# Kernel optimization log

Measured on AMD Instinct MI355X. Metric: run time of the kernel, lower is better.

Reference implementation:

```python
import jax, jax.numpy as jnp
import numpy as np

N_EMBED = 512
E_DIM = 256
BETA = 0.25


def setup_inputs() -> dict:
    key = jax.random.key(0)
    k1, k2 = jax.random.split(key)
    z = jax.random.normal(k1, (32, 16, 16, 16, E_DIM), dtype=jnp.float32)
    embedding = jax.random.normal(k2, (N_EMBED, E_DIM), dtype=jnp.float32)
    return {"z": z, "embedding": embedding}


def reference(z, embedding):
    # Flatten spatial/batch dims: [N, e_dim]
    zf = z.reshape(-1, E_DIM)
    # similarity = ||z||^2 + ||e||^2 - 2 z.e  (squared distances)
    sim = (
        jnp.sum(zf * zf, axis=1, keepdims=True)
        + jnp.sum(embedding * embedding, axis=1)
        - 2.0 * jnp.einsum("bd,nd->bn", zf, embedding)
    )
    # NOTE: original code uses argmax (farthest code) -- faithfully reproduced.
    codebook_idxs = jnp.argmax(sim, axis=-1)
    # histogram side-effect: codebook_hist[idx] += 1
    hist = jnp.zeros((N_EMBED,), dtype=jnp.float32).at[codebook_idxs].add(1.0)
    z_q = embedding[codebook_idxs].reshape(z.shape)
    vq_loss = jnp.mean((z_q - jax.lax.stop_gradient(z)) ** 2)
    commitment_loss = BETA * jnp.mean((jax.lax.stop_gradient(z_q) - z) ** 2)
    # straight-through estimator
    z_q_st = z + jax.lax.stop_gradient(z_q - z)
    return (z_q_st, vq_loss, commitment_loss, codebook_idxs, hist)
```

## Files before the change

### kernel.cpp

```cpp
#include <hip/hip_runtime.h>
#include <hip/hip_bf16.h>

#define D 256
#define NC 512
#define NROWS 131072L

#define OFF_ZQ   0L
#define OFF_VQ   33554432L
#define OFF_CM   33554433L
#define OFF_IDX  33554434L
#define OFF_HIST 33685506L

#define WS_LPART 0
#define WS_HIST  2048
#define WS_E2    2560
#define WS_CNT   3072
#define WS_AMB   3136
#define WS_FIDX  134208
#define WS_BK    265280
#define WS_NEED  (330816L * 4)

#define MARGIN 0.75f

typedef __attribute__((ext_vector_type(8))) short bf16x8;
typedef __attribute__((ext_vector_type(4))) float f32x4;

__device__ __forceinline__ unsigned short f2bf(float f) {
    union { float f; unsigned int u; } a; a.f = f;
    return (unsigned short)((a.u + 0x7FFFu + ((a.u >> 16) & 1u)) >> 16);
}

__global__ void vq_e2(const float* __restrict__ e, float* __restrict__ e2) {
    int c = blockIdx.x;
    int l = threadIdx.x;
    float4 v = *(const float4*)(e + c * D + l * 4);
    float s = v.x * v.x + v.y * v.y + v.z * v.z + v.w * v.w;
    #pragma unroll
    for (int off = 32; off; off >>= 1) s += __shfl_xor(s, off);
    if (l == 0) e2[c] = s;
}

__global__ void vq_convB(const float* __restrict__ e, unsigned short* __restrict__ Bk,
                         float* __restrict__ e2, float* __restrict__ hist,
                         int* __restrict__ acnt) {
    __shared__ float r4[4];
    int code = blockIdx.x, k = threadIdx.x;
    float v = e[code * D + k];
    Bk[((k >> 5) * NC + code) * 32 + (k & 31)] = f2bf(v);
    float s = v * v;
    #pragma unroll
    for (int off = 32; off; off >>= 1) s += __shfl_xor(s, off);
    if ((k & 63) == 0) r4[k >> 6] = s;
    if (k == 0) {
        hist[code] = 0.0f;
        if (code == 0) *acnt = 0;
    }
    __syncthreads();
    if (k == 0) e2[code] = r4[0] + r4[1] + r4[2] + r4[3];
}

__global__ __launch_bounds__(512, 4)
void vq_gemm(const float* __restrict__ z, const unsigned short* __restrict__ Bk,
             const float* __restrict__ e2, int* __restrict__ fidx,
             int* __restrict__ acnt, int* __restrict__ alist) {
    __shared__ __align__(16) unsigned short zh[64 * 264];
    __shared__ float red[64 * 25];

    const int tid = threadIdx.x;
    const int w = tid >> 6, l = tid & 63, q = l >> 4, ln = l & 15;
    const long row0 = (long)blockIdx.x * 64;

    #pragma unroll
    for (int j = 0; j < 8; ++j) {
        int c = j * 512 + tid;
        int row = c >> 6, c4 = (c & 63) * 4;
        float4 av = *(const float4*)(z + (row0 + row) * D + c4);
        *(ushort4*)&zh[row * 264 + c4] =
            make_ushort4(f2bf(av.x), f2bf(av.y), f2bf(av.z), f2bf(av.w));
    }

    const unsigned short* bb = Bk + ((w * 64 + ln) * 32 + q * 8);
    bf16x8 ring[4];
    #pragma unroll
    for (int p = 0; p < 4; ++p)
        ring[p] = *(const bf16x8*)(bb + (p & 7) * (NC * 32) + (p >> 3) * (16 * 32));

    __syncthreads();

    float v1[16], v2[16]; int i1[16];
    #pragma unroll
    for (int k = 0; k < 16; ++k) { v1[k] = -3.0e38f; v2[k] = -3.0e38f; i1[k] = 0; }

    #pragma unroll
    for (int nt = 0; nt < 4; ++nt) {
        const int colc = w * 64 + nt * 16 + ln;
        const float e2v = e2[colc];
        f32x4 acc[4];
        #pragma unroll
        for (int mt = 0; mt < 4; ++mt) acc[mt] = (f32x4){0.f, 0.f, 0.f, 0.f};
        #pragma unroll
        for (int s = 0; s < 8; ++s) {
            const int it = nt * 8 + s;
            bf16x8 b = ring[it & 3];
            if (it + 4 < 32) {
                const int jt = it + 4;
                ring[it & 3] = *(const bf16x8*)(bb + (jt & 7) * (NC * 32) + (jt >> 3) * (16 * 32));
            }
            #pragma unroll
            for (int mt = 0; mt < 4; ++mt) {
                bf16x8 a = *(const bf16x8*)&zh[(mt * 16 + ln) * 264 + s * 32 + q * 8];
                acc[mt] = __builtin_amdgcn_mfma_f32_16x16x32_bf16(a, b, acc[mt], 0, 0, 0);
            }
        }
        #pragma unroll
        for (int mt = 0; mt < 4; ++mt)
            #pragma unroll
            for (int r = 0; r < 4; ++r) {
                const int k = mt * 4 + r;
                float v = fmaf(-2.0f, acc[mt][r], e2v);
                if (v > v1[k]) { v2[k] = v1[k]; v1[k] = v; i1[k] = colc; }
                else v2[k] = fmaxf(v2[k], v);
            }
    }

    #pragma unroll
    for (int k = 0; k < 16; ++k) {
        float v1p = v1[k];
        #pragma unroll
        for (int off = 1; off < 16; off <<= 1) {
            float o1 = __shfl_xor(v1[k], off);
            float o2 = __shfl_xor(v2[k], off);
            v2[k] = fmaxf(fmaxf(v2[k], o2), fminf(v1[k], o1));
            v1[k] = fmaxf(v1[k], o1);
        }
        unsigned long long mm = __ballot(v1p == v1[k]);
        unsigned int gm = (unsigned int)((mm >> (q * 16)) & 0xFFFFULL);
        int src = (q << 4) + (__ffs(gm) - 1);
        int ii = __shfl(i1[k], src);
        if (ln == 0) {
            const int mt = k >> 2, r = k & 3;
            const int rr = mt * 16 + q * 4 + r;
            red[rr * 25 + w * 3 + 0] = v1[k];
            red[rr * 25 + w * 3 + 1] = (float)ii;
            red[rr * 25 + w * 3 + 2] = v2[k];
        }
    }
    __syncthreads();
    if (tid < 64) {
        float v1m = -3.0e38f, v2m = -3.0e38f; int i1m = 0;
        #pragma unroll
        for (int g = 0; g < 8; ++g) {
            float rv1 = red[tid * 25 + g * 3 + 0];
            int   ri  = (int)red[tid * 25 + g * 3 + 1];
            float rv2 = red[tid * 25 + g * 3 + 2];
            if (rv1 > v1m) { v2m = fmaxf(v1m, rv2); v1m = rv1; i1m = ri; }
            else v2m = fmaxf(v2m, rv1);
        }
        fidx[row0 + tid] = i1m;
        int amb = (v1m - v2m < MARGIN) ? 1 : 0;
        unsigned long long m = __ballot(amb);
        int nb = __popcll(m);
        int basep = 0;
        if (tid == 0 && nb) basep = atomicAdd(acnt, nb);
        basep = __shfl(basep, 0);
        if (amb) {
            int pfx = __popcll(m & ((1ULL << tid) - 1ULL));
            alist[basep + pfx] = (int)(row0 + tid);
        }
    }
}

__global__ __launch_bounds__(256, 2)
void vq_refine(const float* __restrict__ z, const float* __restrict__ e,
               const float* __restrict__ e2, const int* __restrict__ acnt,
               const int* __restrict__ alist, int* __restrict__ fidx) {
    __shared__ __align__(16) float z_s[32][D];
    __shared__ __align__(16) float e_s[16][NC + 4];
    __shared__ int rowg[32];
    __shared__ int idx_s[32];
    const int tid = threadIdx.x, lane = tid & 63, w = tid >> 6;
    const int cnt = *acnt;
    for (int g = blockIdx.x; g * 32 < cnt; g += gridDim.x) {
        const int base = g * 32;
        __syncthreads();
        if (tid < 32) rowg[tid] = alist[min(base + tid, cnt - 1)];
        __syncthreads();
        #pragma unroll
        for (int j = 0; j < 8; ++j) {
            int c = j * 256 + tid, rl = c >> 6, c4 = (c & 63) * 4;
            *(float4*)&z_s[rl][c4] = *(const float4*)(z + (long)rowg[rl] * D + c4);
        }
        float acc[8][8];
        #pragma unroll
        for (int r = 0; r < 8; ++r)
            #pragma unroll
            for (int c = 0; c < 8; ++c) acc[r][c] = 0.0f;
        const int r0 = w * 8, c_lo = lane * 4;
        for (int kc = 0; kc < D; kc += 16) {
            __syncthreads();
            #pragma unroll
            for (int p = 0; p < 8; ++p) {
                int c = p * 64 + (tid >> 2), kk4 = (tid & 3) * 4;
                float4 v = *(const float4*)(e + c * D + kc + kk4);
                e_s[kk4 + 0][c] = v.x; e_s[kk4 + 1][c] = v.y;
                e_s[kk4 + 2][c] = v.z; e_s[kk4 + 3][c] = v.w;
            }
            __syncthreads();
            #pragma unroll
            for (int k4 = 0; k4 < 16; k4 += 4) {
                float zr[8][4];
                #pragma unroll
                for (int r = 0; r < 8; ++r) *(float4*)zr[r] = *(const float4*)&z_s[r0 + r][kc + k4];
                #pragma unroll
                for (int kk = 0; kk < 4; ++kk) {
                    float ev[8];
                    *(float4*)&ev[0] = *(const float4*)&e_s[k4 + kk][c_lo];
                    *(float4*)&ev[4] = *(const float4*)&e_s[k4 + kk][c_lo + 256];
                    #pragma unroll
                    for (int r = 0; r < 8; ++r)
                        #pragma unroll
                        for (int c = 0; c < 8; ++c) acc[r][c] = fmaf(zr[r][kk], ev[c], acc[r][c]);
                }
            }
        }
        float e2v[8];
        #pragma unroll
        for (int gg = 0; gg < 2; ++gg)
            #pragma unroll
            for (int i = 0; i < 4; ++i) e2v[gg * 4 + i] = e2[gg * 256 + c_lo + i];
        #pragma unroll
        for (int r = 0; r < 8; ++r) {
            float bvv = -3.0e38f; int bc = 0;
            #pragma unroll
            for (int c = 0; c < 8; ++c) {
                int col = (c >> 2) * 256 + c_lo + (c & 3);
                float v = e2v[c] - 2.0f * acc[r][c];
                if (v > bvv) { bvv = v; bc = col; }
            }
            #pragma unroll
            for (int off = 32; off; off >>= 1) {
                float ov = __shfl_xor(bvv, off); int oc = __shfl_xor(bc, off);
                if (ov > bvv || (ov == bvv && oc < bc)) { bvv = ov; bc = oc; }
            }
            if (lane == 0) idx_s[r0 + r] = bc;
        }
        __syncthreads();
        if (tid < 32 && base + tid < cnt) fidx[rowg[tid]] = idx_s[tid];
    }
}

__global__ __launch_bounds__(256)
void vq_hist(const int* __restrict__ fidx, float* __restrict__ hist) {
    __shared__ int h[NC];
    const int t = threadIdx.x;
    h[t] = 0; h[t + 256] = 0;
    __syncthreads();
    const long base = (long)blockIdx.x * 2048;
    #pragma unroll
    for (int j = 0; j < 8; ++j) {
        long i = base + j * 256 + t;
        atomicAdd(&h[fidx[i]], 1);
    }
    __syncthreads();
    #pragma unroll
    for (int j = 0; j < 2; ++j) {
        int k = j * 256 + t;
        int c = h[k];
        if (c) atomicAdd(&hist[k], (float)c);
    }
}

__global__ __launch_bounds__(256)
void vq_epi(const float* __restrict__ z, const float* __restrict__ e,
            const int* __restrict__ fidx, float* __restrict__ out,
            float* __restrict__ lpart) {
    __shared__ int idxs[64];
    __shared__ float rs[4];
    const int t = threadIdx.x, lane = t & 63, w = t >> 6;
    const long row0 = (long)blockIdx.x * 64;
    if (t < 64) {
        int ix = fidx[row0 + t];
        idxs[t] = ix;
        out[OFF_IDX + row0 + t] = (float)ix;
    }
    __syncthreads();
    float ls = 0.f;
    #pragma unroll 4
    for (int j = 0; j < 16; ++j) {
        const int r = w * 16 + j;
        const long row = row0 + r;
        const int idx = idxs[r];
        float4 zv = *(const float4*)(z + row * D + lane * 4);
        float4 ev = *(const float4*)(e + (long)idx * D + lane * 4);
        float4 dq;
        dq.x = ev.x - zv.x; dq.y = ev.y - zv.y; dq.z = ev.z - zv.z; dq.w = ev.w - zv.w;
        float4 o;
        o.x = zv.x + dq.x; o.y = zv.y + dq.y; o.z = zv.z + dq.z; o.w = zv.w + dq.w;
        *(float4*)(out + OFF_ZQ + row * D + lane * 4) = o;
        ls += dq.x * dq.x + dq.y * dq.y + dq.z * dq.z + dq.w * dq.w;
    }
    #pragma unroll
    for (int off = 32; off; off >>= 1) ls += __shfl_xor(ls, off);
    if (lane == 0) rs[w] = ls;
    __syncthreads();
    if (t == 0) lpart[blockIdx.x] = rs[0] + rs[1] + rs[2] + rs[3];
}

__global__ void vq_fin(const float* __restrict__ ws, float* __restrict__ out) {
    __shared__ float sred[16];
    const int t = threadIdx.x, lane = t & 63, w = t >> 6;
    float s = ws[WS_LPART + t] + ws[WS_LPART + t + 1024];
    #pragma unroll
    for (int off = 32; off; off >>= 1) s += __shfl_xor(s, off);
    if (lane == 0) sred[w] = s;
    __syncthreads();
    if (t == 0) {
        float tot = 0.f;
        #pragma unroll
        for (int i = 0; i < 16; ++i) tot += sred[i];
        float m = tot / 33554432.0f;
        out[OFF_VQ] = m;
        out[OFF_CM] = 0.25f * m;
    }
    if (t < NC) out[OFF_HIST + t] = ws[WS_HIST + t];
}

__global__ __launch_bounds__(256, 2)
void vq_main_fb(const float* __restrict__ z, const float* __restrict__ e,
                const float* __restrict__ e2, float* __restrict__ out,
                float* __restrict__ ws_loss, float* __restrict__ ws_hist) {
    __shared__ __align__(16) float z_s[32][D];
    __shared__ __align__(16) float e_s[16][NC + 4];
    __shared__ int   idx_s[32];
    __shared__ float red_s[4];
    const int tid = threadIdx.x, lane = tid & 63, w = tid >> 6;
    const long row0 = (long)blockIdx.x * 32;
    {
        const float4* zg = (const float4*)(z + row0 * D);
        float4* zs = (float4*)(&z_s[0][0]);
        #pragma unroll
        for (int i = 0; i < 8; ++i) zs[i * 256 + tid] = zg[i * 256 + tid];
    }
    float acc[8][8];
    #pragma unroll
    for (int r = 0; r < 8; ++r)
        #pragma unroll
        for (int c = 0; c < 8; ++c) acc[r][c] = 0.0f;
    const int r0 = w * 8, c_lo = lane * 4;
    for (int kc = 0; kc < D; kc += 16) {
        __syncthreads();
        #pragma unroll
        for (int p = 0; p < 8; ++p) {
            int c = p * 64 + (tid >> 2), kk4 = (tid & 3) * 4;
            float4 v = *(const float4*)(e + c * D + kc + kk4);
            e_s[kk4 + 0][c] = v.x; e_s[kk4 + 1][c] = v.y;
            e_s[kk4 + 2][c] = v.z; e_s[kk4 + 3][c] = v.w;
        }
        __syncthreads();
        #pragma unroll
        for (int k4 = 0; k4 < 16; k4 += 4) {
            float zr[8][4];
            #pragma unroll
            for (int r = 0; r < 8; ++r) *(float4*)zr[r] = *(const float4*)&z_s[r0 + r][kc + k4];
            #pragma unroll
            for (int kk = 0; kk < 4; ++kk) {
                float ev[8];
                *(float4*)&ev[0] = *(const float4*)&e_s[k4 + kk][c_lo];
                *(float4*)&ev[4] = *(const float4*)&e_s[k4 + kk][c_lo + 256];
                #pragma unroll
                for (int r = 0; r < 8; ++r)
                    #pragma unroll
                    for (int c = 0; c < 8; ++c) acc[r][c] = fmaf(zr[r][kk], ev[c], acc[r][c]);
            }
        }
    }
    float e2v[8];
    #pragma unroll
    for (int g = 0; g < 2; ++g)
        #pragma unroll
        for (int i = 0; i < 4; ++i) e2v[g * 4 + i] = e2[g * 256 + c_lo + i];
    #pragma unroll
    for (int r = 0; r < 8; ++r) {
        float bvv = -3.0e38f; int bc = 0;
        #pragma unroll
        for (int c = 0; c < 8; ++c) {
            int col = (c >> 2) * 256 + c_lo + (c & 3);
            float v = e2v[c] - 2.0f * acc[r][c];
            if (v > bvv) { bvv = v; bc = col; }
        }
        #pragma unroll
        for (int off = 32; off; off >>= 1) {
            float ov = __shfl_xor(bvv, off); int oc = __shfl_xor(bc, off);
            if (ov > bvv || (ov == bvv && oc < bc)) { bvv = ov; bc = oc; }
        }
        if (lane == 0) idx_s[r] = bc;
    }
    __syncthreads();
    if (tid < 32) {
        int bc = idx_s[tid];
        out[OFF_IDX + row0 + tid] = (float)bc;
        atomicAdd(&ws_hist[bc], 1.0f);
    }
    float lsum = 0.0f;
    for (int r = 0; r < 32; ++r) {
        int idx = idx_s[r];
        float ev = e[idx * D + tid];
        float zv = z_s[r][tid];
        float dq = ev - zv;
        out[OFF_ZQ + (row0 + r) * D + tid] = zv + dq;
        lsum += dq * dq;
    }
    #pragma unroll
    for (int off = 32; off; off >>= 1) lsum += __shfl_xor(lsum, off);
    if (lane == 0) red_s[w] = lsum;
    __syncthreads();
    if (tid == 0) atomicAdd(ws_loss, red_s[0] + red_s[1] + red_s[2] + red_s[3]);
}

__global__ void vq_init_fb(float* __restrict__ ws) {
    int t = threadIdx.x;
    if (t < 513) ws[t] = 0.0f;
}
__global__ void vq_fin_fb(const float* __restrict__ ws, float* __restrict__ out) {
    int t = blockIdx.x * blockDim.x + threadIdx.x;
    if (t < NC) out[OFF_HIST + t] = ws[1 + t];
    if (t == NC) {
        float m = ws[0] / 33554432.0f;
        out[OFF_VQ] = m; out[OFF_CM] = 0.25f * m;
    }
}

extern "C" void kernel_launch(void* const* d_in, const int* in_sizes, int n_in,
                              void* d_out, int out_size, void* d_ws, size_t ws_size,
                              hipStream_t stream) {
    const float* z = (const float*)d_in[0];
    const float* e = (const float*)d_in[1];
    float* out = (float*)d_out;
    float* ws  = (float*)d_ws;

    if (ws_size >= (size_t)WS_NEED) {
        float* lpart = ws + WS_LPART;
        float* hist  = ws + WS_HIST;
        float* e2    = ws + WS_E2;
        int*   acnt  = (int*)(ws + WS_CNT);
        int*   alist = (int*)(ws + WS_AMB);
        int*   fidx  = (int*)(ws + WS_FIDX);
        unsigned short* Bk = (unsigned short*)(ws + WS_BK);

        vq_convB<<<NC, 256, 0, stream>>>(e, Bk, e2, hist, acnt);
        vq_gemm<<<2048, 512, 0, stream>>>(z, Bk, e2, fidx, acnt, alist);
        vq_refine<<<512, 256, 0, stream>>>(z, e, e2, acnt, alist, fidx);
        vq_hist<<<64, 256, 0, stream>>>(fidx, hist);
        vq_epi<<<2048, 256, 0, stream>>>(z, e, fidx, out, lpart);
        vq_fin<<<1, 1024, 0, stream>>>(ws, out);
    } else {
        float* ws_loss = ws;
        float* ws_hist = ws + 1;
        float* ws_e2   = ws + 513;
        vq_init_fb<<<1, 1024, 0, stream>>>(ws);
        vq_e2<<<NC, 64, 0, stream>>>(e, ws_e2);
        vq_main_fb<<<4096, 256, 0, stream>>>(z, e, ws_e2, out, ws_loss, ws_hist);
        vq_fin_fb<<<3, 256, 0, stream>>>(ws, out);
    }
}
```

Measured before the change: 382.6 us.

## Hold z fragments in registers with a 2x4 warp tile; fuse hist and final reduction

The GEMM kernel stops staging z through LDS. Each wave now loads its 32 rows of z straight into registers as bf16 MFMA A-fragments and covers 128 codes, using a 2x4 wave grid in place of 8 waves each covering 64 codes over all 64 rows. This removes the LDS writes and reads and the block barrier before the MFMA loop, at the cost of higher register pressure (launch bounds lowered to 3 blocks) and more streaming of B per wave. Separately, the histogram and final loss kernels are merged into one launch that uses a last-block-done atomic counter, which saves one kernel launch.

```diff
diff --git a/kernel.cpp b/kernel.cpp
--- a/kernel.cpp
+++ b/kernel.cpp
@@ -15,6 +15,7 @@
 #define WS_HIST  2048
 #define WS_E2    2560
 #define WS_CNT   3072
+#define WS_DONE  3073
 #define WS_AMB   3136
 #define WS_FIDX  134208
 #define WS_BK    265280
@@ -42,7 +43,7 @@
 
 __global__ void vq_convB(const float* __restrict__ e, unsigned short* __restrict__ Bk,
                          float* __restrict__ e2, float* __restrict__ hist,
-                         int* __restrict__ acnt) {
+                         int* __restrict__ acnt, int* __restrict__ done) {
     __shared__ float r4[4];
     int code = blockIdx.x, k = threadIdx.x;
     float v = e[code * D + k];
@@ -53,78 +54,84 @@
     if ((k & 63) == 0) r4[k >> 6] = s;
     if (k == 0) {
         hist[code] = 0.0f;
-        if (code == 0) *acnt = 0;
+        if (code == 0) { *acnt = 0; *done = 0; }
     }
     __syncthreads();
     if (k == 0) e2[code] = r4[0] + r4[1] + r4[2] + r4[3];
 }
 
-__global__ __launch_bounds__(512, 4)
+__global__ __launch_bounds__(512, 3)
 void vq_gemm(const float* __restrict__ z, const unsigned short* __restrict__ Bk,
              const float* __restrict__ e2, int* __restrict__ fidx,
              int* __restrict__ acnt, int* __restrict__ alist) {
-    __shared__ __align__(16) unsigned short zh[64 * 264];
-    __shared__ float red[64 * 25];
+    __shared__ float red[64 * 13];
 
     const int tid = threadIdx.x;
     const int w = tid >> 6, l = tid & 63, q = l >> 4, ln = l & 15;
+    const int wm = w >> 2, wn = w & 3;
     const long row0 = (long)blockIdx.x * 64;
-
-    #pragma unroll
-    for (int j = 0; j < 8; ++j) {
-        int c = j * 512 + tid;
-        int row = c >> 6, c4 = (c & 63) * 4;
-        float4 av = *(const float4*)(z + (row0 + row) * D + c4);
-        *(ushort4*)&zh[row * 264 + c4] =
-            make_ushort4(f2bf(av.x), f2bf(av.y), f2bf(av.z), f2bf(av.w));
-    }
-
-    const unsigned short* bb = Bk + ((w * 64 + ln) * 32 + q * 8);
+    const long rowW = row0 + wm * 32;
+
+    bf16x8 af[2][8];
+    #pragma unroll
+    for (int mt = 0; mt < 2; ++mt) {
+        const float* zp = z + (rowW + mt * 16 + ln) * D + q * 8;
+        #pragma unroll
+        for (int s = 0; s < 8; ++s) {
+            float4 a0 = *(const float4*)(zp + s * 32);
+            float4 a1 = *(const float4*)(zp + s * 32 + 4);
+            bf16x8 t;
+            t[0] = (short)f2bf(a0.x); t[1] = (short)f2bf(a0.y);
+            t[2] = (short)f2bf(a0.z); t[3] = (short)f2bf(a0.w);
+            t[4] = (short)f2bf(a1.x); t[5] = (short)f2bf(a1.y);
+            t[6] = (short)f2bf(a1.z); t[7] = (short)f2bf(a1.w);
+            af[mt][s] = t;
+        }
+    }
+
+    float e2v[8];
+    #pragma unroll
+    for (int nt = 0; nt < 8; ++nt) e2v[nt] = e2[wn * 128 + nt * 16 + ln];
+
+    const unsigned short* bb = Bk + ((wn * 128 + ln) * 32 + q * 8);
     bf16x8 ring[4];
     #pragma unroll
     for (int p = 0; p < 4; ++p)
         ring[p] = *(const bf16x8*)(bb + (p & 7) * (NC * 32) + (p >> 3) * (16 * 32));
 
-    __syncthreads();
-
-    float v1[16], v2[16]; int i1[16];
-    #pragma unroll
-    for (int k = 0; k < 16; ++k) { v1[k] = -3.0e38f; v2[k] = -3.0e38f; i1[k] = 0; }
-
-    #pragma unroll
-    for (int nt = 0; nt < 4; ++nt) {
-        const int colc = w * 64 + nt * 16 + ln;
-        const float e2v = e2[colc];
-        f32x4 acc[4];
-        #pragma unroll
-        for (int mt = 0; mt < 4; ++mt) acc[mt] = (f32x4){0.f, 0.f, 0.f, 0.f};
+    float v1[8], v2[8]; int i1[8];
+    #pragma unroll
+    for (int k = 0; k < 8; ++k) { v1[k] = -3.0e38f; v2[k] = -3.0e38f; i1[k] = 0; }
+
+    #pragma unroll
+    for (int nt = 0; nt < 8; ++nt) {
+        f32x4 acc0 = (f32x4){0.f, 0.f, 0.f, 0.f};
+        f32x4 acc1 = (f32x4){0.f, 0.f, 0.f, 0.f};
         #pragma unroll
         for (int s = 0; s < 8; ++s) {
             const int it = nt * 8 + s;
             bf16x8 b = ring[it & 3];
-            if (it + 4 < 32) {
+            if (it + 4 < 64) {
                 const int jt = it + 4;
                 ring[it & 3] = *(const bf16x8*)(bb + (jt & 7) * (NC * 32) + (jt >> 3) * (16 * 32));
             }
-            #pragma unroll
-            for (int mt = 0; mt < 4; ++mt) {
-                bf16x8 a = *(const bf16x8*)&zh[(mt * 16 + ln) * 264 + s * 32 + q * 8];
-                acc[mt] = __builtin_amdgcn_mfma_f32_16x16x32_bf16(a, b, acc[mt], 0, 0, 0);
-            }
-        }
-        #pragma unroll
-        for (int mt = 0; mt < 4; ++mt)
-            #pragma unroll
-            for (int r = 0; r < 4; ++r) {
-                const int k = mt * 4 + r;
-                float v = fmaf(-2.0f, acc[mt][r], e2v);
-                if (v > v1[k]) { v2[k] = v1[k]; v1[k] = v; i1[k] = colc; }
-                else v2[k] = fmaxf(v2[k], v);
-            }
-    }
-
-    #pragma unroll
-    for (int k = 0; k < 16; ++k) {
+            acc0 = __builtin_amdgcn_mfma_f32_16x16x32_bf16(af[0][s], b, acc0, 0, 0, 0);
+            acc1 = __builtin_amdgcn_mfma_f32_16x16x32_bf16(af[1][s], b, acc1, 0, 0, 0);
+        }
+        const int colc = wn * 128 + nt * 16 + ln;
+        #pragma unroll
+        for (int r = 0; r < 4; ++r) {
+            float v = fmaf(-2.0f, acc0[r], e2v[nt]);
+            if (v > v1[r]) { v2[r] = v1[r]; v1[r] = v; i1[r] = colc; }
+            else v2[r] = fmaxf(v2[r], v);
+            float u = fmaf(-2.0f, acc1[r], e2v[nt]);
+            if (u > v1[4 + r]) { v2[4 + r] = v1[4 + r]; v1[4 + r] = u; i1[4 + r] = colc; }
+            else v2[4 + r] = fmaxf(v2[4 + r], u);
+        }
+    }
+
+    #pragma unroll
+    for (int k = 0; k < 8; ++k) {
         float v1p = v1[k];
         #pragma unroll
         for (int off = 1; off < 16; off <<= 1) {
@@ -139,20 +146,20 @@
         int ii = __shfl(i1[k], src);
         if (ln == 0) {
             const int mt = k >> 2, r = k & 3;
-            const int rr = mt * 16 + q * 4 + r;
-            red[rr * 25 + w * 3 + 0] = v1[k];
-            red[rr * 25 + w * 3 + 1] = (float)ii;
-            red[rr * 25 + w * 3 + 2] = v2[k];
+            const int rr = wm * 32 + mt * 16 + q * 4 + r;
+            red[rr * 13 + wn * 3 + 0] = v1[k];
+            red[rr * 13 + wn * 3 + 1] = (float)ii;
+            red[rr * 13 + wn * 3 + 2] = v2[k];
         }
     }
     __syncthreads();
     if (tid < 64) {
         float v1m = -3.0e38f, v2m = -3.0e38f; int i1m = 0;
         #pragma unroll
-        for (int g = 0; g < 8; ++g) {
-            float rv1 = red[tid * 25 + g * 3 + 0];
-            int   ri  = (int)red[tid * 25 + g * 3 + 1];
-            float rv2 = red[tid * 25 + g * 3 + 2];
+        for (int g = 0; g < 4; ++g) {
+            float rv1 = red[tid * 13 + g * 3 + 0];
+            int   ri  = (int)red[tid * 13 + g * 3 + 1];
+            float rv2 = red[tid * 13 + g * 3 + 2];
             if (rv1 > v1m) { v2m = fmaxf(v1m, rv2); v1m = rv1; i1m = ri; }
             else v2m = fmaxf(v2m, rv1);
         }
@@ -250,27 +257,6 @@
 }
 
 __global__ __launch_bounds__(256)
-void vq_hist(const int* __restrict__ fidx, float* __restrict__ hist) {
-    __shared__ int h[NC];
-    const int t = threadIdx.x;
-    h[t] = 0; h[t + 256] = 0;
-    __syncthreads();
-    const long base = (long)blockIdx.x * 2048;
-    #pragma unroll
-    for (int j = 0; j < 8; ++j) {
-        long i = base + j * 256 + t;
-        atomicAdd(&h[fidx[i]], 1);
-    }
-    __syncthreads();
-    #pragma unroll
-    for (int j = 0; j < 2; ++j) {
-        int k = j * 256 + t;
-        int c = h[k];
-        if (c) atomicAdd(&hist[k], (float)c);
-    }
-}
-
-__global__ __launch_bounds__(256)
 void vq_epi(const float* __restrict__ z, const float* __restrict__ e,
             const int* __restrict__ fidx, float* __restrict__ out,
             float* __restrict__ lpart) {
@@ -306,23 +292,48 @@
     if (t == 0) lpart[blockIdx.x] = rs[0] + rs[1] + rs[2] + rs[3];
 }
 
-__global__ void vq_fin(const float* __restrict__ ws, float* __restrict__ out) {
-    __shared__ float sred[16];
+__global__ __launch_bounds__(256)
+void vq_hist(const int* __restrict__ fidx, const float* __restrict__ lpart,
+             float* __restrict__ hist, int* __restrict__ done,
+             float* __restrict__ out) {
+    __shared__ int h[NC];
+    __shared__ float sred[4];
+    __shared__ int lastf;
     const int t = threadIdx.x, lane = t & 63, w = t >> 6;
-    float s = ws[WS_LPART + t] + ws[WS_LPART + t + 1024];
+    h[t] = 0; h[t + 256] = 0;
+    __syncthreads();
+    const long base = (long)blockIdx.x * 2048;
+    #pragma unroll
+    for (int j = 0; j < 8; ++j) {
+        long i = base + j * 256 + t;
+        atomicAdd(&h[fidx[i]], 1);
+    }
+    __syncthreads();
+    #pragma unroll
+    for (int j = 0; j < 2; ++j) {
+        int k = j * 256 + t;
+        int c = h[k];
+        if (c) atomicAdd(&hist[k], (float)c);
+    }
+    __threadfence();
+    if (t == 0) lastf = (atomicAdd(done, 1) == 63);
+    __syncthreads();
+    if (!lastf) return;
+    __threadfence();
+    out[OFF_HIST + t]       = atomicAdd(&hist[t], 0.0f);
+    out[OFF_HIST + 256 + t] = atomicAdd(&hist[t + 256], 0.0f);
+    float s = 0.f;
+    #pragma unroll
+    for (int j = 0; j < 8; ++j) s += lpart[j * 256 + t];
     #pragma unroll
     for (int off = 32; off; off >>= 1) s += __shfl_xor(s, off);
     if (lane == 0) sred[w] = s;
     __syncthreads();
     if (t == 0) {
-        float tot = 0.f;
-        #pragma unroll
-        for (int i = 0; i < 16; ++i) tot += sred[i];
-        float m = tot / 33554432.0f;
+        float m = (sred[0] + sred[1] + sred[2] + sred[3]) / 33554432.0f;
         out[OFF_VQ] = m;
         out[OFF_CM] = 0.25f * m;
     }
-    if (t < NC) out[OFF_HIST + t] = ws[WS_HIST + t];
 }
 
 __global__ __launch_bounds__(256, 2)
@@ -443,16 +454,16 @@
         float* hist  = ws + WS_HIST;
         float* e2    = ws + WS_E2;
         int*   acnt  = (int*)(ws + WS_CNT);
+        int*   done  = (int*)(ws + WS_DONE);
         int*   alist = (int*)(ws + WS_AMB);
         int*   fidx  = (int*)(ws + WS_FIDX);
         unsigned short* Bk = (unsigned short*)(ws + WS_BK);
 
-        vq_convB<<<NC, 256, 0, stream>>>(e, Bk, e2, hist, acnt);
+        vq_convB<<<NC, 256, 0, stream>>>(e, Bk, e2, hist, acnt, done);
         vq_gemm<<<2048, 512, 0, stream>>>(z, Bk, e2, fidx, acnt, alist);
         vq_refine<<<512, 256, 0, stream>>>(z, e, e2, acnt, alist, fidx);
-        vq_hist<<<64, 256, 0, stream>>>(fidx, hist);
         vq_epi<<<2048, 256, 0, stream>>>(z, e, fidx, out, lpart);
-        vq_fin<<<1, 1024, 0, stream>>>(ws, out);
+        vq_hist<<<64, 256, 0, stream>>>(fidx, lpart, hist, done, out);
     } else {
         float* ws_loss = ws;
         float* ws_hist = ws + 1;
```

Result: slower. 442.2 us (+15.6%).
